# Kernel optimization log

Measured on AMD Instinct MI355X. Metric: run time of the kernel, lower is better.

## Reference

```python
import jax, jax.numpy as jnp
import numpy as np

B, L, HID, H = 2, 384, 512, 8
D = HID // H  # head_dim = 64


def setup_inputs() -> dict:
    key = jax.random.key(0)
    ks = jax.random.split(key, 16)
    s = 0.02
    return {
        "query": jax.random.normal(ks[0], (B, L, HID), jnp.float32),
        "key_": jax.random.normal(ks[1], (B, L, HID), jnp.float32),
        "value": jax.random.normal(ks[2], (B, L, HID), jnp.float32),
        "mask": jnp.ones((B, 1, 1, L), jnp.int32),
        # fc_q/k/v/o: nn.Linear(hid_dim, hid_dim)
        "Wq": jax.random.normal(ks[3], (HID, HID), jnp.float32) * s,
        "bq": jnp.zeros((HID,), jnp.float32),
        "Wk": jax.random.normal(ks[4], (HID, HID), jnp.float32) * s,
        "bk": jnp.zeros((HID,), jnp.float32),
        "Wv": jax.random.normal(ks[5], (HID, HID), jnp.float32) * s,
        "bv": jnp.zeros((HID,), jnp.float32),
        "Wo": jax.random.normal(ks[6], (HID, HID), jnp.float32) * s,
        "bo": jnp.zeros((HID,), jnp.float32),
        # additive-attention score MLP: W1, W2: Linear(D, D); v: Linear(D, 1)
        "W1": jax.random.normal(ks[7], (D, D), jnp.float32) * s,
        "b1": jnp.zeros((D,), jnp.float32),
        "W2": jax.random.normal(ks[8], (D, D), jnp.float32) * s,
        "b2": jnp.zeros((D,), jnp.float32),
        "vw": jax.random.normal(ks[9], (1, D), jnp.float32) * s,
        "vb": jnp.zeros((1,), jnp.float32),
    }


def reference(query, key_, value, mask, Wq, bq, Wk, bk, Wv, bv, Wo, bo,
              W1, b1, W2, b2, vw, vb):
    b = query.shape[0]
    # projections (torch Linear: x @ W.T + b)
    Q = query @ Wq.T + bq
    K = key_ @ Wk.T + bk
    V = value @ Wv.T + bv
    # [b, h, l, d]
    def split_heads(x):
        return x.reshape(b, -1, H, D).transpose(0, 2, 1, 3)
    Q, K, V = split_heads(Q), split_heads(K), split_heads(V)
    # additive (Bahdanau-style) score: v^T tanh(W1 q + W2 k)
    tQ = Q @ W1.T + b1            # [b, h, lq, d]
    tK = K @ W2.T + b2            # [b, h, lk, d]
    e = jnp.tanh(tQ[:, :, :, None, :] + tK[:, :, None, :, :])  # [b,h,lq,lk,d]
    energy = jnp.einsum('bhqkd,d->bhqk', e, vw[0]) + vb[0]      # [b,h,lq,lk]
    energy = jnp.where(mask == 0, jnp.float32(-1e10), energy)
    attention = jax.nn.softmax(energy, axis=-1)
    x = jnp.einsum('bhqk,bhkd->bhqd', attention, V)  # dropout p=0 (eval)
    x = x.transpose(0, 2, 1, 3).reshape(b, -1, HID)
    x = x @ Wo.T + bo
    return x, attention
```

## Files before the change

kernel.cpp:

```cpp
#include <hip/hip_runtime.h>

#define BATCH 2
#define LSEQ 384
#define NHID 512
#define NH 8
#define DH 64
#define BH (BATCH*NH)
#define XELEMS ((size_t)768 * NHID)
#define TQ 8
#define QTILES (LSEQ/TQ)

typedef unsigned short ushort_t;
typedef __attribute__((ext_vector_type(8))) short bf16x8;
typedef __attribute__((ext_vector_type(4))) float f32x4;

__device__ __forceinline__ float bf2f(ushort_t u) {
    unsigned int v = ((unsigned int)u) << 16;
    return __uint_as_float(v);
}
__device__ __forceinline__ ushort_t f2bf(float f) {
    unsigned int u = __float_as_uint(f);
    unsigned int lsb = (u >> 16) & 1u;
    u += 0x7fffu + lsb;
    return (ushort_t)(u >> 16);
}
__device__ __forceinline__ unsigned pk_bf16(float a, float b) {
    unsigned ua = __float_as_uint(a), ub = __float_as_uint(b);
    ua += 0x7fffu + ((ua >> 16) & 1u);
    ub += 0x7fffu + ((ub >> 16) & 1u);
    return __builtin_amdgcn_perm(ub, ua, 0x07060302);
}
__device__ __forceinline__ float ld1(const void* p, size_t i, int f) {
    return f ? ((const float*)p)[i] : bf2f(((const ushort_t*)p)[i]);
}
__device__ __forceinline__ float4 ld4(const void* p, size_t i, int f) {
    if (f) return ((const float4*)p)[i >> 2];
    ushort4 u = ((const ushort4*)p)[i >> 2];
    return make_float4(bf2f(u.x), bf2f(u.y), bf2f(u.z), bf2f(u.w));
}
__device__ __forceinline__ int block_detect(const unsigned int* q, int* cnt) {
    int t = threadIdx.x;
    if (t == 0) *cnt = 0;
    __syncthreads();
    int n = blockDim.x < 256 ? blockDim.x : 256;
    if (t < n) {
        unsigned int elo = (q[t] >> 7) & 0xFFu;
        if (elo >= 100u && elo <= 150u) atomicAdd(cnt, 1);
    }
    __syncthreads();
    return (*cnt * 2 > n) ? 0 : 1;
}
__device__ __forceinline__ uint4 packu4(float4 a, float4 b) {
    uint4 r;
    r.x = pk_bf16(a.x, a.y); r.y = pk_bf16(a.z, a.w);
    r.z = pk_bf16(b.x, b.y); r.w = pk_bf16(b.z, b.w);
    return r;
}
__device__ __forceinline__ bf16x8 pack_bf8(float4 a, float4 b) {
    union { uint4 u; bf16x8 v; } r;
    r.u = packu4(a, b);
    return r.v;
}

#define OFF_ETQ   16
#define OFF_ETK   (16 + 393216)
#define OFF_VH    (16 + 2*393216)
#define OFF_XH    (16 + 3*393216)

#define LDSTR 72

__global__ __launch_bounds__(128) void gemm_qkv(
    const void* qp, const void* kp, const void* vp,
    const void* Wqp, const void* Wkp, const void* Wvp,
    const void* W1p, const void* W2p,
    const void* bqp, const void* bkp, const void* b1p, const void* b2p,
    const void* bvp, float* __restrict__ ws)
{
    __shared__ int s_cnt;
    __shared__ ushort_t smA[32 * LDSTR];
    __shared__ ushort_t smB[64 * LDSTR];
    __shared__ float biasF[64];
    const int f = block_detect((const unsigned int*)qp, &s_cnt);

    const int mode = blockIdx.z;
    const void* A = (mode == 0) ? qp : (mode == 1) ? kp : vp;
    const void* W = (mode == 0) ? Wqp : (mode == 1) ? Wkp : Wvp;
    const void* W1x = (mode == 1) ? W2p : W1p;

    const int h    = blockIdx.x;
    const int col0 = h * 64;
    const int row0 = blockIdx.y * 32;
    const int t = threadIdx.x;
    const int w = t >> 6, l16 = t & 15, quad = (t & 63) >> 4;

    if (t < 64) {
        if (mode == 2) {
            biasF[t] = ld1(bvp, col0 + t, f);
        } else {
            const void* b1x = (mode == 1) ? b2p : b1p;
            const void* bx  = (mode == 1) ? bkp : bqp;
            float s = ld1(b1x, t, f);
            for (int j = 0; j < 64; j++)
                s = fmaf(ld1(W1x, (size_t)t * 64 + j, f), ld1(bx, h * 64 + j, f), s);
            biasF[t] = s;
        }
    }

    const int arow = t >> 2, acol = (t & 3) * 16;
    const int brow = t >> 1, bcol = (t & 1) * 32;
    const size_t abase = (size_t)(row0 + arow) * 512 + acol;
    const size_t bbase = (size_t)(col0 + brow) * 512 + bcol;

    float4 a4[4], b4[8];
    #pragma unroll
    for (int i = 0; i < 4; i++) a4[i] = ld4(A, abase + i * 4, f);
    #pragma unroll
    for (int i = 0; i < 8; i++) b4[i] = ld4(W, bbase + i * 4, f);

    f32x4 acc[4];
    #pragma unroll
    for (int nt = 0; nt < 4; nt++) acc[nt] = (f32x4){0.f, 0.f, 0.f, 0.f};

    for (int k0 = 0; k0 < 512; k0 += 64) {
        __syncthreads();
        *reinterpret_cast<uint4*>(&smA[arow * LDSTR + acol])     = packu4(a4[0], a4[1]);
        *reinterpret_cast<uint4*>(&smA[arow * LDSTR + acol + 8]) = packu4(a4[2], a4[3]);
        *reinterpret_cast<uint4*>(&smB[brow * LDSTR + bcol])      = packu4(b4[0], b4[1]);
        *reinterpret_cast<uint4*>(&smB[brow * LDSTR + bcol + 8])  = packu4(b4[2], b4[3]);
        *reinterpret_cast<uint4*>(&smB[brow * LDSTR + bcol + 16]) = packu4(b4[4], b4[5]);
        *reinterpret_cast<uint4*>(&smB[brow * LDSTR + bcol + 24]) = packu4(b4[6], b4[7]);
        __syncthreads();
        if (k0 + 64 < 512) {
            #pragma unroll
            for (int i = 0; i < 4; i++) a4[i] = ld4(A, abase + k0 + 64 + i * 4, f);
            #pragma unroll
            for (int i = 0; i < 8; i++) b4[i] = ld4(W, bbase + k0 + 64 + i * 4, f);
        }
        #pragma unroll
        for (int kk = 0; kk < 2; kk++) {
            bf16x8 af = *reinterpret_cast<const bf16x8*>(
                &smA[(w * 16 + l16) * LDSTR + kk * 32 + quad * 8]);
            #pragma unroll
            for (int nt = 0; nt < 4; nt++) {
                bf16x8 bfr = *reinterpret_cast<const bf16x8*>(
                    &smB[(nt * 16 + l16) * LDSTR + kk * 32 + quad * 8]);
                acc[nt] = __builtin_amdgcn_mfma_f32_16x16x32_bf16(af, bfr, acc[nt], 0, 0, 0);
            }
        }
    }

    const int b  = (row0 >= LSEQ) ? 1 : 0;
    const int lbase = row0 - b * LSEQ + w * 16;
    const int bh = b * NH + h;

    if (mode == 2) {
        float* Out = ws + OFF_VH;
        #pragma unroll
        for (int nt = 0; nt < 4; nt++) {
            int d = l16 + nt * 16;
            float bi = biasF[d];
            #pragma unroll
            for (int r = 0; r < 4; r++) {
                int l = lbase + quad * 4 + r;
                Out[(size_t)(bh * LSEQ + l) * 64 + d] = acc[nt][r] + bi;
            }
        }
    } else {
        #pragma unroll
        for (int nt = 0; nt < 4; nt++)
            #pragma unroll
            for (int r = 0; r < 4; r++)
                smA[(w * 16 + quad * 4 + r) * LDSTR + l16 + nt * 16] =
                    f2bf(acc[nt][r]);
        f32x4 acc2[4];
        #pragma unroll
        for (int nt = 0; nt < 4; nt++) acc2[nt] = (f32x4){0.f, 0.f, 0.f, 0.f};
        #pragma unroll
        for (int kk = 0; kk < 2; kk++) {
            bf16x8 af2 = *reinterpret_cast<const bf16x8*>(
                &smA[(w * 16 + l16) * LDSTR + kk * 32 + quad * 8]);
            #pragma unroll
            for (int nt = 0; nt < 4; nt++) {
                int od = nt * 16 + l16, j0 = kk * 32 + quad * 8;
                float4 wa = ld4(W1x, (size_t)od * 64 + j0, f);
                float4 wb = ld4(W1x, (size_t)od * 64 + j0 + 4, f);
                bf16x8 bfw = pack_bf8(wa, wb);
                acc2[nt] = __builtin_amdgcn_mfma_f32_16x16x32_bf16(af2, bfw, acc2[nt], 0, 0, 0);
            }
        }
        float* Out = ws + ((mode == 0) ? OFF_ETQ : OFF_ETK);
        #pragma unroll
        for (int nt = 0; nt < 4; nt++) {
            int d = l16 + nt * 16;
            float bi = biasF[d];
            #pragma unroll
            for (int r = 0; r < 4; r++) {
                int l = lbase + quad * 4 + r;
                Out[(size_t)(bh * LSEQ + l) * 64 + d] =
                    __expf(2.f * (acc2[nt][r] + bi));
            }
        }
    }
}

__global__ __launch_bounds__(384, 6) void attn_kernel(
    const void* qp, const void* vwp, const void* vbp,
    const float* __restrict__ ws_in, float* __restrict__ ws,
    const int* __restrict__ mask, void* __restrict__ dout)
{
    __shared__ int s_cnt;
    const int f = block_detect((const unsigned int*)qp, &s_cnt);

    const float* Etq = ws_in + OFF_ETQ;
    const float* Etk = ws_in + OFF_ETK;
    const float* Vh  = ws_in + OFF_VH;
    float* Xh = ws + OFF_XH;

    const int bid = blockIdx.x;
    const int qt = bid % QTILES;
    const int bh = bid / QTILES;
    const int q0 = qt * TQ;
    const int b  = bh >> 3;
    const int h  = bh & 7;
    const int t  = threadIdx.x;
    const int wave = t >> 6;

    __shared__ __align__(16) float etq8[64][TQ];
    __shared__ float vws[64];
    __shared__ float ps[TQ][LSEQ];
    __shared__ float red[6][TQ][16][4];
    __shared__ float rsum[TQ][6];
    __shared__ float s_vb;

    for (int i = t; i < TQ * 64; i += 384) {
        int qi = i >> 6, d = i & 63;
        etq8[d][qi] = Etq[(size_t)(bh * LSEQ + q0 + qi) * 64 + d];
    }
    if (t < 64) {
        float v = ld1(vwp, t, f);
        vws[t] = v;
        #pragma unroll
        for (int off = 32; off > 0; off >>= 1) v += __shfl_xor(v, off, 64);
        if (t == 0) s_vb = ld1(vbp, 0, f) + v;
    }
    const int mok = mask[b * LSEQ + t];
    __syncthreads();
    const float vbSum = s_vb;

    float e2[TQ] = {0.f, 0.f, 0.f, 0.f, 0.f, 0.f, 0.f, 0.f};
    const float* ekrow = Etk + (size_t)(bh * LSEQ + t) * 64;
    #pragma unroll 4
    for (int dv = 0; dv < 16; dv++) {
        float4 ek4 = *reinterpret_cast<const float4*>(ekrow + dv * 4);
        #pragma unroll
        for (int j = 0; j < 4; j++) {
            int d = dv * 4 + j;
            float ekv = (j == 0) ? ek4.x : (j == 1) ? ek4.y : (j == 2) ? ek4.z : ek4.w;
            float4 eqA = *reinterpret_cast<const float4*>(&etq8[d][0]);
            float4 eqB = *reinterpret_cast<const float4*>(&etq8[d][4]);
            float wv = vws[d];
            e2[0] = fmaf(wv, __builtin_amdgcn_rcpf(fmaf(eqA.x, ekv, 1.0f)), e2[0]);
            e2[1] = fmaf(wv, __builtin_amdgcn_rcpf(fmaf(eqA.y, ekv, 1.0f)), e2[1]);
            e2[2] = fmaf(wv, __builtin_amdgcn_rcpf(fmaf(eqA.z, ekv, 1.0f)), e2[2]);
            e2[3] = fmaf(wv, __builtin_amdgcn_rcpf(fmaf(eqA.w, ekv, 1.0f)), e2[3]);
            e2[4] = fmaf(wv, __builtin_amdgcn_rcpf(fmaf(eqB.x, ekv, 1.0f)), e2[4]);
            e2[5] = fmaf(wv, __builtin_amdgcn_rcpf(fmaf(eqB.y, ekv, 1.0f)), e2[5]);
            e2[6] = fmaf(wv, __builtin_amdgcn_rcpf(fmaf(eqB.z, ekv, 1.0f)), e2[6]);
            e2[7] = fmaf(wv, __builtin_amdgcn_rcpf(fmaf(eqB.w, ekv, 1.0f)), e2[7]);
        }
    }

    float p[TQ];
    #pragma unroll
    for (int qi = 0; qi < TQ; qi++) {
        float en = fmaf(-2.0f, e2[qi], vbSum);
        if (mok == 0) en = -1e10f;
        p[qi] = __expf(en);
        float s = p[qi];
        #pragma unroll
        for (int off = 32; off > 0; off >>= 1) s += __shfl_xor(s, off, 64);
        if ((t & 63) == 0) rsum[qi][wave] = s;
    }
    __syncthreads();
    #pragma unroll
    for (int qi = 0; qi < TQ; qi++) {
        float gs = rsum[qi][0] + rsum[qi][1] + rsum[qi][2] +
                   rsum[qi][3] + rsum[qi][4] + rsum[qi][5];
        p[qi] *= 1.0f / gs;
        ps[qi][t] = p[qi];
        size_t aidx = XELEMS + (size_t)(bh * LSEQ + q0 + qi) * LSEQ + t;
        if (f) ((float*)dout)[aidx] = p[qi];
        else   ((ushort_t*)dout)[aidx] = f2bf(p[qi]);
    }
    __syncthreads();

    const int dq = t & 15;
    const int ksub = t >> 4;
    const float* vb4 = Vh + (size_t)bh * LSEQ * 64 + dq * 4;
    float4 acc[TQ];
    #pragma unroll
    for (int qi = 0; qi < TQ; qi++) acc[qi] = make_float4(0.f, 0.f, 0.f, 0.f);
    for (int kk = ksub; kk < LSEQ; kk += 24) {
        float4 v4 = *reinterpret_cast<const float4*>(vb4 + (size_t)kk * 64);
        #pragma unroll
        for (int qi = 0; qi < TQ; qi++) {
            float pq = ps[qi][kk];
            acc[qi].x = fmaf(pq, v4.x, acc[qi].x);
            acc[qi].y = fmaf(pq, v4.y, acc[qi].y);
            acc[qi].z = fmaf(pq, v4.z, acc[qi].z);
            acc[qi].w = fmaf(pq, v4.w, acc[qi].w);
        }
    }
    #pragma unroll
    for (int qi = 0; qi < TQ; qi++) {
        #pragma unroll
        for (int off = 16; off <= 32; off <<= 1) {
            acc[qi].x += __shfl_xor(acc[qi].x, off, 64);
            acc[qi].y += __shfl_xor(acc[qi].y, off, 64);
            acc[qi].z += __shfl_xor(acc[qi].z, off, 64);
            acc[qi].w += __shfl_xor(acc[qi].w, off, 64);
        }
    }
    if ((t & 63) < 16) {
        #pragma unroll
        for (int qi = 0; qi < TQ; qi++) {
            red[wave][qi][dq][0] = acc[qi].x;
            red[wave][qi][dq][1] = acc[qi].y;
            red[wave][qi][dq][2] = acc[qi].z;
            red[wave][qi][dq][3] = acc[qi].w;
        }
    }
    __syncthreads();
    if (t < 256) {
        int d = t & 63;
        #pragma unroll
        for (int half = 0; half < 2; half++) {
            int qi = (t >> 6) + half * 4;
            float sx = 0.f;
            #pragma unroll
            for (int w = 0; w < 6; w++) sx += red[w][qi][d >> 2][d & 3];
            Xh[((size_t)(b * LSEQ + q0 + qi) * NH + h) * 64 + d] = sx;
        }
    }
}

__global__ __launch_bounds__(128) void gemm_out(
    const void* qp, const void* Wop, const void* bop,
    const float* __restrict__ ws_in, void* __restrict__ dout)
{
    __shared__ int s_cnt;
    __shared__ ushort_t smA[32 * LDSTR];
    __shared__ ushort_t smB[64 * LDSTR];
    __shared__ float biasF[64];
    const int f = block_detect((const unsigned int*)qp, &s_cnt);

    const float* Xh = ws_in + OFF_XH;
    const int col0 = blockIdx.x * 64;
    const int row0 = blockIdx.y * 32;
    const int t = threadIdx.x;
    const int w = t >> 6, l16 = t & 15, quad = (t & 63) >> 4;

    if (t < 64) biasF[t] = ld1(bop, col0 + t, f);

    const int arow = t >> 2, acol = (t & 3) * 16;
    const int brow = t >> 1, bcol = (t & 1) * 32;
    const float* Ab = Xh + (size_t)(row0 + arow) * 512 + acol;
    const size_t bbase = (size_t)(col0 + brow) * 512 + bcol;

    float4 a4[4], b4[8];
    #pragma unroll
    for (int i = 0; i < 4; i++) a4[i] = *reinterpret_cast<const float4*>(Ab + i * 4);
    #pragma unroll
    for (int i = 0; i < 8; i++) b4[i] = ld4(Wop, bbase + i * 4, f);

    f32x4 acc[4];
    #pragma unroll
    for (int nt = 0; nt < 4; nt++) acc[nt] = (f32x4){0.f, 0.f, 0.f, 0.f};

    for (int k0 = 0; k0 < 512; k0 += 64) {
        __syncthreads();
        *reinterpret_cast<uint4*>(&smA[arow * LDSTR + acol])     = packu4(a4[0], a4[1]);
        *reinterpret_cast<uint4*>(&smA[arow * LDSTR + acol + 8]) = packu4(a4[2], a4[3]);
        *reinterpret_cast<uint4*>(&smB[brow * LDSTR + bcol])      = packu4(b4[0], b4[1]);
        *reinterpret_cast<uint4*>(&smB[brow * LDSTR + bcol + 8])  = packu4(b4[2], b4[3]);
        *reinterpret_cast<uint4*>(&smB[brow * LDSTR + bcol + 16]) = packu4(b4[4], b4[5]);
        *reinterpret_cast<uint4*>(&smB[brow * LDSTR + bcol + 24]) = packu4(b4[6], b4[7]);
        __syncthreads();
        if (k0 + 64 < 512) {
            #pragma unroll
            for (int i = 0; i < 4; i++)
                a4[i] = *reinterpret_cast<const float4*>(Ab + k0 + 64 + i * 4);
            #pragma unroll
            for (int i = 0; i < 8; i++) b4[i] = ld4(Wop, bbase + k0 + 64 + i * 4, f);
        }
        #pragma unroll
        for (int kk = 0; kk < 2; kk++) {
            bf16x8 af = *reinterpret_cast<const bf16x8*>(
                &smA[(w * 16 + l16) * LDSTR + kk * 32 + quad * 8]);
            #pragma unroll
            for (int nt = 0; nt < 4; nt++) {
                bf16x8 bfr = *reinterpret_cast<const bf16x8*>(
                    &smB[(nt * 16 + l16) * LDSTR + kk * 32 + quad * 8]);
                acc[nt] = __builtin_amdgcn_mfma_f32_16x16x32_bf16(af, bfr, acc[nt], 0, 0, 0);
            }
        }
    }

    #pragma unroll
    for (int nt = 0; nt < 4; nt++) {
        int n = col0 + l16 + nt * 16;
        float bi = biasF[l16 + nt * 16];
        #pragma unroll
        for (int r = 0; r < 4; r++) {
            int m = row0 + w * 16 + quad * 4 + r;
            float c = acc[nt][r] + bi;
            size_t idx = (size_t)m * 512 + n;
            if (f) ((float*)dout)[idx] = c;
            else   ((ushort_t*)dout)[idx] = f2bf(c);
        }
    }
}

extern "C" void kernel_launch(void* const* d_in, const int* in_sizes, int n_in,
                              void* d_out, int out_size, void* d_ws, size_t ws_size,
                              hipStream_t stream)
{
    const void* qp = d_in[0];
    const void* kp = d_in[1];
    const void* vp = d_in[2];
    const int* mask = (const int*)d_in[3];
    const void* Wqp = d_in[4];  const void* bqp = d_in[5];
    const void* Wkp = d_in[6];  const void* bkp = d_in[7];
    const void* Wvp = d_in[8];  const void* bvp = d_in[9];
    const void* Wop = d_in[10]; const void* bop = d_in[11];
    const void* W1p = d_in[12]; const void* b1p = d_in[13];
    const void* W2p = d_in[14]; const void* b2p = d_in[15];
    const void* vwp = d_in[16]; const void* vbp = d_in[17];

    float* ws = (float*)d_ws;

    gemm_qkv<<<dim3(8, 24, 3), 128, 0, stream>>>(qp, kp, vp, Wqp, Wkp, Wvp,
                                                 W1p, W2p, bqp, bkp, b1p, b2p,
                                                 bvp, ws);
    attn_kernel<<<BH * QTILES, 384, 0, stream>>>(qp, vwp, vbp, ws, ws, mask, d_out);
    gemm_out<<<dim3(8, 24, 1), 128, 0, stream>>>(qp, Wop, bop, ws, d_out);
}
```

Before: 165.3 us.

## Combine four reciprocal terms into one rcp and use packed f32x2 math

The score loop previously took one reciprocal per (q,k,d) term, computing w/(1+a*b). It now pre-divides the Etq tile by the vw weights and rewrites each term as 1/(c+a'*b) with c=1/w. Four such terms are summed as a single fraction, so one rcp covers four dimensions, and the arithmetic uses packed two-wide float vectors. This cuts transcendental throughput cost, but risks overflow, underflow or loss of precision in the product of four denominators, and breaks if any vw weight is zero.

```diff
diff --git a/kernel.cpp b/kernel.cpp
--- a/kernel.cpp
+++ b/kernel.cpp
@@ -13,6 +13,7 @@
 typedef unsigned short ushort_t;
 typedef __attribute__((ext_vector_type(8))) short bf16x8;
 typedef __attribute__((ext_vector_type(4))) float f32x4;
+typedef __attribute__((ext_vector_type(2))) float f32x2;
 
 __device__ __forceinline__ float bf2f(ushort_t u) {
     unsigned int v = ((unsigned int)u) << 16;
@@ -226,7 +227,7 @@
     const int wave = t >> 6;
 
     __shared__ __align__(16) float etq8[64][TQ];
-    __shared__ float vws[64];
+    __shared__ f32x2 cws2[64];
     __shared__ float ps[TQ][LSEQ];
     __shared__ float red[6][TQ][16][4];
     __shared__ float rsum[TQ][6];
@@ -234,11 +235,13 @@
 
     for (int i = t; i < TQ * 64; i += 384) {
         int qi = i >> 6, d = i & 63;
-        etq8[d][qi] = Etq[(size_t)(bh * LSEQ + q0 + qi) * 64 + d];
+        float wv = ld1(vwp, d, f);
+        etq8[d][qi] = Etq[(size_t)(bh * LSEQ + q0 + qi) * 64 + d] / wv;
     }
     if (t < 64) {
         float v = ld1(vwp, t, f);
-        vws[t] = v;
+        float r = 1.0f / v;
+        cws2[t] = (f32x2){r, r};
         #pragma unroll
         for (int off = 32; off > 0; off >>= 1) v += __shfl_xor(v, off, 64);
         if (t == 0) s_vb = ld1(vbp, 0, f) + v;
@@ -247,33 +250,50 @@
     __syncthreads();
     const float vbSum = s_vb;
 
-    float e2[TQ] = {0.f, 0.f, 0.f, 0.f, 0.f, 0.f, 0.f, 0.f};
+    f32x2 e2p0 = {0.f, 0.f}, e2p1 = {0.f, 0.f};
+    f32x2 e2p2 = {0.f, 0.f}, e2p3 = {0.f, 0.f};
     const float* ekrow = Etk + (size_t)(bh * LSEQ + t) * 64;
-    #pragma unroll 4
+    #pragma unroll 2
     for (int dv = 0; dv < 16; dv++) {
         float4 ek4 = *reinterpret_cast<const float4*>(ekrow + dv * 4);
-        #pragma unroll
-        for (int j = 0; j < 4; j++) {
-            int d = dv * 4 + j;
-            float ekv = (j == 0) ? ek4.x : (j == 1) ? ek4.y : (j == 2) ? ek4.z : ek4.w;
-            float4 eqA = *reinterpret_cast<const float4*>(&etq8[d][0]);
-            float4 eqB = *reinterpret_cast<const float4*>(&etq8[d][4]);
-            float wv = vws[d];
-            e2[0] = fmaf(wv, __builtin_amdgcn_rcpf(fmaf(eqA.x, ekv, 1.0f)), e2[0]);
-            e2[1] = fmaf(wv, __builtin_amdgcn_rcpf(fmaf(eqA.y, ekv, 1.0f)), e2[1]);
-            e2[2] = fmaf(wv, __builtin_amdgcn_rcpf(fmaf(eqA.z, ekv, 1.0f)), e2[2]);
-            e2[3] = fmaf(wv, __builtin_amdgcn_rcpf(fmaf(eqA.w, ekv, 1.0f)), e2[3]);
-            e2[4] = fmaf(wv, __builtin_amdgcn_rcpf(fmaf(eqB.x, ekv, 1.0f)), e2[4]);
-            e2[5] = fmaf(wv, __builtin_amdgcn_rcpf(fmaf(eqB.y, ekv, 1.0f)), e2[5]);
-            e2[6] = fmaf(wv, __builtin_amdgcn_rcpf(fmaf(eqB.z, ekv, 1.0f)), e2[6]);
-            e2[7] = fmaf(wv, __builtin_amdgcn_rcpf(fmaf(eqB.w, ekv, 1.0f)), e2[7]);
-        }
-    }
+        const int d0 = dv * 4;
+        const f32x2 vcA = cws2[d0];
+        const f32x2 vcB = cws2[d0 + 1];
+        const f32x2 vcC = cws2[d0 + 2];
+        const f32x2 vcD = cws2[d0 + 3];
+        const f32x2 ekA = {ek4.x, ek4.x};
+        const f32x2 ekB = {ek4.y, ek4.y};
+        const f32x2 ekC = {ek4.z, ek4.z};
+        const f32x2 ekD = {ek4.w, ek4.w};
+#define ESTEP(EP, i) { \
+        f32x2 ua = __builtin_elementwise_fma( \
+            *reinterpret_cast<const f32x2*>(&etq8[d0][2*(i)]),     ekA, vcA); \
+        f32x2 ub = __builtin_elementwise_fma( \
+            *reinterpret_cast<const f32x2*>(&etq8[d0 + 1][2*(i)]), ekB, vcB); \
+        f32x2 uc = __builtin_elementwise_fma( \
+            *reinterpret_cast<const f32x2*>(&etq8[d0 + 2][2*(i)]), ekC, vcC); \
+        f32x2 ud = __builtin_elementwise_fma( \
+            *reinterpret_cast<const f32x2*>(&etq8[d0 + 3][2*(i)]), ekD, vcD); \
+        f32x2 pab = ua * ub, pcd = uc * ud; \
+        f32x2 P = pab * pcd; \
+        f32x2 num = __builtin_elementwise_fma(ua + ub, pcd, (uc + ud) * pab); \
+        f32x2 rP; \
+        rP.x = __builtin_amdgcn_rcpf(P.x); \
+        rP.y = __builtin_amdgcn_rcpf(P.y); \
+        EP = __builtin_elementwise_fma(num, rP, EP); }
+        ESTEP(e2p0, 0)
+        ESTEP(e2p1, 1)
+        ESTEP(e2p2, 2)
+        ESTEP(e2p3, 3)
+#undef ESTEP
+    }
+    const float ex[TQ] = {e2p0.x, e2p0.y, e2p1.x, e2p1.y,
+                          e2p2.x, e2p2.y, e2p3.x, e2p3.y};
 
     float p[TQ];
     #pragma unroll
     for (int qi = 0; qi < TQ; qi++) {
-        float en = fmaf(-2.0f, e2[qi], vbSum);
+        float en = fmaf(-2.0f, ex[qi], vbSum);
         if (mok == 0) en = -1e10f;
         p[qi] = __expf(en);
         float s = p[qi];
```

New measurement: 159.2 us. -3.7%, faster.
